# Kernel tuning notes

Hardware: AMD Instinct MI355X
Metric: run time of the kernel (lower is better)

The kernel has to match this reference:

```python
import jax, jax.numpy as jnp
import numpy as np

B, S, D, H = 4, 1024, 1024, 16
DK = D // H
NEG = -1e9


def setup_inputs() -> dict:
    key = jax.random.key(0)
    ks = jax.random.split(key, 8)
    inp = {
        "query": jax.random.normal(ks[0], (B, S, D), dtype=jnp.float32),
        "key": jax.random.normal(ks[1], (B, S, D), dtype=jnp.float32),
        "value": jax.random.normal(ks[2], (B, S, D), dtype=jnp.float32),
        "mask": jax.random.randint(ks[3], (B, S, S), 0, 2, dtype=jnp.int32),
        # bias-free Linear weights, torch layout [out, in]; y = x @ W.T
        "Wq": jax.random.normal(ks[4], (D, D), dtype=jnp.float32) / np.sqrt(D),
        "Wk": jax.random.normal(ks[5], (D, D), dtype=jnp.float32) / np.sqrt(D),
        "Wv": jax.random.normal(ks[6], (D, D), dtype=jnp.float32) / np.sqrt(D),
        "Wo": jax.random.normal(ks[7], (D, D), dtype=jnp.float32) / np.sqrt(D),
    }
    return inp


def _split_heads(x):
    # [B, S, D] -> [B, H, S, DK]
    return x.reshape(B, -1, H, DK).transpose(0, 2, 1, 3)


def reference(query, key, value, mask, Wq, Wk, Wv, Wo):
    q = _split_heads(query @ Wq.T)
    k = _split_heads(key @ Wk.T)
    v = _split_heads(value @ Wv.T)
    scores = jnp.einsum("bhqd,bhkd->bhqk", q, k) / jnp.sqrt(jnp.float32(DK))
    scores = jnp.where(mask[:, None, :, :] == 0, NEG, scores)
    p_attn = jax.nn.softmax(scores, axis=-1)
    x = jnp.einsum("bhqk,bhkd->bhqd", p_attn, v)
    x = x.transpose(0, 2, 1, 3).reshape(B, -1, D)
    # dropout p=0.0 (eval-equivalent): identity
    return x @ Wo.T
```

## Files before the change

kernel.cpp:

```cpp
#include <hip/hip_runtime.h>

#define BB 4
#define SS 1024
#define DD 1024
#define HH 16
#define DKK 64
#define MM (BB*SS)

typedef __bf16 bf16;
typedef __bf16 bf16x8 __attribute__((ext_vector_type(8)));
typedef float f32x4 __attribute__((ext_vector_type(4)));
typedef float f32x16 __attribute__((ext_vector_type(16)));

__device__ __forceinline__ f32x4 mfma16(bf16x8 a, bf16x8 b, f32x4 c) {
  return __builtin_amdgcn_mfma_f32_16x16x32_bf16(a, b, c, 0, 0, 0);
}
__device__ __forceinline__ f32x16 mfma32(bf16x8 a, bf16x8 b, f32x16 c) {
  return __builtin_amdgcn_mfma_f32_32x32x16_bf16(a, b, c, 0, 0, 0);
}
__device__ __forceinline__ float fexp2(float x) {
  return __builtin_amdgcn_exp2f(x);
}
__device__ __forceinline__ void gld_lds16(const bf16* g, bf16* l) {
  __builtin_amdgcn_global_load_lds(
      (const __attribute__((address_space(1))) void*)g,
      (__attribute__((address_space(3))) void*)l, 16, 0, 0);
}

__global__ __launch_bounds__(256)
void k_cvt7(const float* __restrict__ s0, const float* __restrict__ s1,
            const float* __restrict__ s2, const float* __restrict__ s3,
            const float* __restrict__ s4, const float* __restrict__ s5,
            const float* __restrict__ s6,
            bf16* __restrict__ d0, bf16* __restrict__ d1, bf16* __restrict__ d2,
            bf16* __restrict__ d3, bf16* __restrict__ d4, bf16* __restrict__ d5,
            bf16* __restrict__ d6) {
  const int t = blockIdx.y;
  const float* s = (t == 0) ? s0 : (t == 1) ? s1 : (t == 2) ? s2
                 : (t == 3) ? s3 : (t == 4) ? s4 : (t == 5) ? s5 : s6;
  bf16* d = (t == 0) ? d0 : (t == 1) ? d1 : (t == 2) ? d2
          : (t == 3) ? d3 : (t == 4) ? d4 : (t == 5) ? d5 : d6;
  const int n = (t < 3) ? (MM * DD) : (DD * DD);
  const int i0 = (blockIdx.x * 256 + threadIdx.x) * 8;
  if (i0 >= n) return;
  const f32x4 a = *(const f32x4*)(s + i0);
  const f32x4 b = *(const f32x4*)(s + i0 + 4);
  bf16x8 o;
#pragma unroll
  for (int j = 0; j < 4; ++j) { o[j] = (bf16)a[j]; o[4 + j] = (bf16)b[j]; }
  *(bf16x8*)(d + i0) = o;
}

__global__ __launch_bounds__(256) void k_mask_bits(const int* __restrict__ mask,
                                                   unsigned* __restrict__ bits) {
  const int row = blockIdx.x;
  const int tid = threadIdx.x;
  const int lane = tid & 63, wv = tid >> 6;
#pragma unroll
  for (int it = 0; it < 4; ++it) {
    const int base = it * 256 + wv * 64;
    const int col = base + lane;
    unsigned long long bal = __ballot(mask[(size_t)row * SS + col] != 0);
    if (lane == 0) {
      bits[(size_t)row * 32 + (base >> 5)] = (unsigned)bal;
      bits[(size_t)row * 32 + (base >> 5) + 1] = (unsigned)(bal >> 32);
    }
  }
}

#define QSCALE 0.1803368801111204f

template<int AF32, int CF32>
__device__ __forceinline__ void gemm_body(const void* __restrict__ Ap,
                                          const float* __restrict__ Wp,
                                          void* __restrict__ Cp,
                                          int Mtot, int N, int K, int blk,
                                          float oscale) {
  __shared__ bf16 Al[128 * 40];
  __shared__ bf16 Bl[128 * 40];
  const int tid = threadIdx.x;
  const int lane = tid & 63;
  const int l15 = lane & 15, l4 = lane >> 4;
  const int wv = tid >> 6;
  const int nbm = Mtot >> 7;
  const int bm = blk % nbm, bn = blk / nbm;
  const size_t m0 = (size_t)bm << 7, n0 = (size_t)bn << 7;
  const int wr = (wv >> 1) << 6, wc = (wv & 1) << 6;
  const int srow = tid >> 2, scol = (tid & 3) << 3;

  f32x4 acc[4][4];
#pragma unroll
  for (int i = 0; i < 4; ++i)
#pragma unroll
    for (int j = 0; j < 4; ++j) acc[i][j] = f32x4{0.f, 0.f, 0.f, 0.f};

  for (int k0 = 0; k0 < K; k0 += 32) {
#pragma unroll
    for (int c = 0; c < 2; ++c) {
      const int row = (c << 6) + srow;
      bf16x8 av;
      if (AF32) {
        const float* s = (const float*)Ap + (m0 + row) * (size_t)K + k0 + scol;
        f32x4 v0 = *(const f32x4*)s;
        f32x4 v1 = *(const f32x4*)(s + 4);
#pragma unroll
        for (int j = 0; j < 4; ++j) { av[j] = (bf16)v0[j]; av[4 + j] = (bf16)v1[j]; }
      } else {
        av = *(const bf16x8*)((const bf16*)Ap + (m0 + row) * (size_t)K + k0 + scol);
      }
      *(bf16x8*)&Al[row * 40 + scol] = av;

      const float* ws_ = Wp + (n0 + row) * (size_t)K + k0 + scol;
      f32x4 w0 = *(const f32x4*)ws_;
      f32x4 w1 = *(const f32x4*)(ws_ + 4);
      bf16x8 wv8;
#pragma unroll
      for (int j = 0; j < 4; ++j) { wv8[j] = (bf16)w0[j]; wv8[4 + j] = (bf16)w1[j]; }
      *(bf16x8*)&Bl[row * 40 + scol] = wv8;
    }
    __syncthreads();

    bf16x8 af[4], bfv[4];
#pragma unroll
    for (int t = 0; t < 4; ++t) {
      af[t]  = *(const bf16x8*)&Al[(wr + t * 16 + l15) * 40 + l4 * 8];
      bfv[t] = *(const bf16x8*)&Bl[(wc + t * 16 + l15) * 40 + l4 * 8];
    }
    __builtin_amdgcn_s_setprio(1);
#pragma unroll
    for (int mt = 0; mt < 4; ++mt)
#pragma unroll
      for (int nt = 0; nt < 4; ++nt)
        acc[mt][nt] = mfma16(af[mt], bfv[nt], acc[mt][nt]);
    __builtin_amdgcn_s_setprio(0);
    __syncthreads();
  }

#pragma unroll
  for (int mt = 0; mt < 4; ++mt)
#pragma unroll
    for (int nt = 0; nt < 4; ++nt)
#pragma unroll
      for (int r = 0; r < 4; ++r) {
        const size_t row = m0 + wr + mt * 16 + l4 * 4 + r;
        const size_t col = n0 + wc + nt * 16 + l15;
        if (CF32) ((float*)Cp)[row * N + col] = acc[mt][nt][r];
        else      ((bf16*)Cp)[row * N + col] = (bf16)(acc[mt][nt][r] * oscale);
      }
}

__global__ __launch_bounds__(256)
void k_gemm_qkv(const float* __restrict__ A0, const float* __restrict__ A1,
                const float* __restrict__ A2, const float* __restrict__ W0,
                const float* __restrict__ W1, const float* __restrict__ W2,
                bf16* __restrict__ C0, bf16* __restrict__ C1, bf16* __restrict__ C2) {
  const int z = blockIdx.z;
  const float* A = (z == 0) ? A0 : (z == 1) ? A1 : A2;
  const float* W = (z == 0) ? W0 : (z == 1) ? W1 : W2;
  bf16* C = (z == 0) ? C0 : (z == 1) ? C1 : C2;
  const float sc = (z == 0) ? QSCALE : 1.0f;
  gemm_body<1, 0>(A, W, C, MM, DD, DD, blockIdx.x, sc);
}

__global__ __launch_bounds__(256)
void k_gemm_out(const bf16* __restrict__ A, const float* __restrict__ W,
                float* __restrict__ C) {
  gemm_body<0, 1>(A, W, C, MM, DD, DD, blockIdx.x, 1.0f);
}

__global__ __launch_bounds__(256)
void k_gemm_qkv_b16(const bf16* __restrict__ A0, const bf16* __restrict__ A1,
                    const bf16* __restrict__ A2, const bf16* __restrict__ W0,
                    const bf16* __restrict__ W1, const bf16* __restrict__ W2,
                    bf16* __restrict__ C0, bf16* __restrict__ C1,
                    bf16* __restrict__ C2) {
  __shared__ bf16 Al[128 * 32];
  __shared__ bf16 Bl[128 * 32];
  const int z = blockIdx.z;
  const bf16* A = (z == 0) ? A0 : (z == 1) ? A1 : A2;
  const bf16* W = (z == 0) ? W0 : (z == 1) ? W1 : W2;
  bf16* C = (z == 0) ? C0 : (z == 1) ? C1 : C2;
  const float oscale = (z == 0) ? QSCALE : 1.0f;

  const int tid = threadIdx.x, lane = tid & 63, w = tid >> 6;
  const int l15 = lane & 15, l4 = lane >> 4;
  const int bm = blockIdx.x & 31, bn = blockIdx.x >> 5;
  const size_t m0 = (size_t)bm << 7, n0 = (size_t)bn << 7;
  const int wr = (w >> 1) << 6, wc = (w & 1) << 6;
  const int srow = w * 32 + (lane >> 2);
  const int scol = (lane & 3) << 3;

  f32x4 acc[4][4];
#pragma unroll
  for (int i = 0; i < 4; ++i)
#pragma unroll
    for (int j = 0; j < 4; ++j) acc[i][j] = f32x4{0.f, 0.f, 0.f, 0.f};

  for (int k0 = 0; k0 < DD; k0 += 32) {
    const bf16* ga = A + (m0 + srow) * (size_t)DD + k0 + scol;
    const bf16* gb = W + (n0 + srow) * (size_t)DD + k0 + scol;
    gld_lds16(ga,            &Al[(w * 32) * 32]);
    gld_lds16(ga + 16 * DD,  &Al[(w * 32 + 16) * 32]);
    gld_lds16(gb,            &Bl[(w * 32) * 32]);
    gld_lds16(gb + 16 * DD,  &Bl[(w * 32 + 16) * 32]);
    __syncthreads();

    bf16x8 af[4], bfv[4];
#pragma unroll
    for (int t = 0; t < 4; ++t) {
      af[t]  = *(const bf16x8*)&Al[(wr + t * 16 + l15) * 32 + l4 * 8];
      bfv[t] = *(const bf16x8*)&Bl[(wc + t * 16 + l15) * 32 + l4 * 8];
    }
#pragma unroll
    for (int mt = 0; mt < 4; ++mt)
#pragma unroll
      for (int nt = 0; nt < 4; ++nt)
        acc[mt][nt] = mfma16(af[mt], bfv[nt], acc[mt][nt]);
    __syncthreads();
  }

#pragma unroll
  for (int mt = 0; mt < 4; ++mt)
#pragma unroll
    for (int nt = 0; nt < 4; ++nt)
#pragma unroll
      for (int r = 0; r < 4; ++r) {
        const size_t row = m0 + wr + mt * 16 + l4 * 4 + r;
        const size_t col = n0 + wc + nt * 16 + l15;
        C[row * DD + col] = (bf16)(acc[mt][nt][r] * oscale);
      }
}

__global__ __launch_bounds__(256)
void k_gemm_out_b16(const bf16* __restrict__ A, const bf16* __restrict__ W,
                    float* __restrict__ C) {
  __shared__ bf16 Al[128 * 32];
  __shared__ bf16 Bl[128 * 32];
  const int tid = threadIdx.x, lane = tid & 63, w = tid >> 6;
  const int l15 = lane & 15, l4 = lane >> 4;
  const int bm = blockIdx.x & 31, bn = blockIdx.x >> 5;
  const size_t m0 = (size_t)bm << 7, n0 = (size_t)bn << 7;
  const int wr = (w >> 1) << 6, wc = (w & 1) << 6;
  const int srow = w * 32 + (lane >> 2);
  const int scol = (lane & 3) << 3;

  f32x4 acc[4][4];
#pragma unroll
  for (int i = 0; i < 4; ++i)
#pragma unroll
    for (int j = 0; j < 4; ++j) acc[i][j] = f32x4{0.f, 0.f, 0.f, 0.f};

  for (int k0 = 0; k0 < DD; k0 += 32) {
    const bf16* ga = A + (m0 + srow) * (size_t)DD + k0 + scol;
    const bf16* gb = W + (n0 + srow) * (size_t)DD + k0 + scol;
    gld_lds16(ga,            &Al[(w * 32) * 32]);
    gld_lds16(ga + 16 * DD,  &Al[(w * 32 + 16) * 32]);
    gld_lds16(gb,            &Bl[(w * 32) * 32]);
    gld_lds16(gb + 16 * DD,  &Bl[(w * 32 + 16) * 32]);
    __syncthreads();

    bf16x8 af[4], bfv[4];
#pragma unroll
    for (int t = 0; t < 4; ++t) {
      af[t]  = *(const bf16x8*)&Al[(wr + t * 16 + l15) * 32 + l4 * 8];
      bfv[t] = *(const bf16x8*)&Bl[(wc + t * 16 + l15) * 32 + l4 * 8];
    }
#pragma unroll
    for (int mt = 0; mt < 4; ++mt)
#pragma unroll
      for (int nt = 0; nt < 4; ++nt)
        acc[mt][nt] = mfma16(af[mt], bfv[nt], acc[mt][nt]);
    __syncthreads();
  }

#pragma unroll
  for (int mt = 0; mt < 4; ++mt)
#pragma unroll
    for (int nt = 0; nt < 4; ++nt)
#pragma unroll
      for (int r = 0; r < 4; ++r) {
        const size_t row = m0 + wr + mt * 16 + l4 * 4 + r;
        const size_t col = n0 + wc + nt * 16 + l15;
        C[row * DD + col] = acc[mt][nt][r];
      }
}

__global__ __launch_bounds__(256)
void k_attn(const bf16* __restrict__ Qw, const bf16* __restrict__ Kw,
            const bf16* __restrict__ Vw, const unsigned* __restrict__ mb,
            bf16* __restrict__ Xw) {
  __shared__ union {
    bf16 v[4][2048];
    struct { float o[64 * 67]; float ml[4][2][64];
             float inv[64]; float mst[64]; } m;
  } sh;
  const int tid = threadIdx.x, lane = tid & 63, w = tid >> 6;
  const int l31 = lane & 31, hi = lane >> 5;
  const unsigned bid = blockIdx.x;
  const unsigned wg = (bid & 7) * 128 + (bid >> 3);
  const int bh = wg >> 4, qblk = wg & 15;
  const int h = bh & 15, b = bh >> 4;
  const int q0 = qblk * 64;

  bf16x8 qf[2][4];
#pragma unroll
  for (int qt = 0; qt < 2; ++qt) {
    const bf16* Qb = Qw + (size_t)(b * SS + q0 + qt * 32 + l31) * DD + h * 64 + hi * 8;
#pragma unroll
    for (int kt = 0; kt < 4; ++kt) qf[qt][kt] = *(const bf16x8*)(Qb + kt * 16);
  }
  const bf16* Kg = Kw + (size_t)(b * SS) * DD + h * 64 + hi * 8;
  const bf16* Vg = Vw + (size_t)(b * SS) * DD + h * 64;
  const unsigned* mrow0 = mb + (size_t)(b * SS + q0 + l31) * 32 + w * 8;
  const unsigned* mrow1 = mrow0 + 32 * 32;

  const int grow = lane >> 3;
  const int gcol = (lane & 7) * 8;
  const int kvw = w << 8;
  bf16* Vst = sh.v[w];

  f32x16 aco[2][2];
#pragma unroll
  for (int qt = 0; qt < 2; ++qt)
#pragma unroll
    for (int dt = 0; dt < 2; ++dt)
#pragma unroll
      for (int r = 0; r < 16; ++r) aco[qt][dt][r] = 0.f;
  float mx[2] = { -3e38f, -3e38f }, ssum[2] = { 0.f, 0.f };

  for (int t = 0; t < 8; ++t) {
    const int kv0 = kvw + t * 32;
#pragma unroll
    for (int i_ = 0; i_ < 4; ++i_)
      gld_lds16(Vg + (size_t)(kv0 + i_ * 8 + grow) * DD + gcol, Vst + i_ * 512);
    bf16x8 kf[4];
    {
      const bf16* kp = Kg + (size_t)(kv0 + l31) * DD;
#pragma unroll
      for (int kt = 0; kt < 4; ++kt) kf[kt] = *(const bf16x8*)(kp + kt * 16);
    }
    const unsigned mw0 = mrow0[t], mw1 = mrow1[t];

    bf16x8 va[2][2];
    union { bf16x8 v; int q[4]; } pa0[2], pa1[2];
    float psum[2];

#pragma unroll
    for (int qt = 0; qt < 2; ++qt) {
      f32x16 s;
#pragma unroll
      for (int r = 0; r < 16; ++r) s[r] = 0.f;
      __builtin_amdgcn_s_setprio(1);
#pragma unroll
      for (int kt = 0; kt < 4; ++kt) s = mfma32(kf[kt], qf[qt][kt], s);
      __builtin_amdgcn_s_setprio(0);

      const unsigned mw = qt ? mw1 : mw0;
      float p[16];
#pragma unroll
      for (int r = 0; r < 16; ++r) {
        const int pos = (r & 3) + 8 * (r >> 2) + 4 * hi;
        p[r] = ((mw >> pos) & 1) ? s[r] : -1e9f;
      }
      float t0 = fmaxf(p[0], p[1]),  t1 = fmaxf(p[2], p[3]);
      float t2 = fmaxf(p[4], p[5]),  t3 = fmaxf(p[6], p[7]);
      float t4 = fmaxf(p[8], p[9]),  t5 = fmaxf(p[10], p[11]);
      float t6 = fmaxf(p[12], p[13]), t7 = fmaxf(p[14], p[15]);
      float rm = fmaxf(fmaxf(fmaxf(t0, t1), fmaxf(t2, t3)),
                       fmaxf(fmaxf(t4, t5), fmaxf(t6, t7)));
      rm = fmaxf(rm, __shfl_xor(rm, 32));
      if (!__all(rm <= mx[qt] + 8.0f)) {
        const float mn = fmaxf(mx[qt], rm);
        const float scal = fexp2(mx[qt] - mn);
        mx[qt] = mn; ssum[qt] *= scal;
#pragma unroll
        for (int dt = 0; dt < 2; ++dt)
#pragma unroll
          for (int r = 0; r < 16; ++r) aco[qt][dt][r] *= scal;
      }
#pragma unroll
      for (int r = 0; r < 16; ++r) p[r] = fexp2(p[r] - mx[qt]);
      {
        float a0 = (p[0] + p[1]) + (p[2] + p[3]);
        float a1 = (p[4] + p[5]) + (p[6] + p[7]);
        float a2 = (p[8] + p[9]) + (p[10] + p[11]);
        float a3 = (p[12] + p[13]) + (p[14] + p[15]);
        psum[qt] = (a0 + a1) + (a2 + a3);
      }
      ssum[qt] += psum[qt];
      int dpk[8];
#pragma unroll
      for (int i = 0; i < 8; ++i) {
        union { bf16 hh[2]; int v; } u;
        u.hh[0] = (bf16)p[2 * i]; u.hh[1] = (bf16)p[2 * i + 1];
        dpk[i] = u.v;
      }
      const int sa = hi ? dpk[0] : dpk[2], sb = hi ? dpk[1] : dpk[3];
      const int sc_ = hi ? dpk[4] : dpk[6], sd = hi ? dpk[5] : dpk[7];
      const int ra = __shfl_xor(sa, 32), rb = __shfl_xor(sb, 32);
      const int rc = __shfl_xor(sc_, 32), rd = __shfl_xor(sd, 32);
      pa0[qt].q[0] = hi ? ra : dpk[0];  pa0[qt].q[1] = hi ? rb : dpk[1];
      pa0[qt].q[2] = hi ? dpk[2] : ra;  pa0[qt].q[3] = hi ? dpk[3] : rb;
      pa1[qt].q[0] = hi ? rc : dpk[4];  pa1[qt].q[1] = hi ? rd : dpk[5];
      pa1[qt].q[2] = hi ? dpk[6] : rc;  pa1[qt].q[3] = hi ? dpk[7] : rd;

      if (qt == 0) {
        asm volatile("s_waitcnt vmcnt(0)" ::: "memory");
        __builtin_amdgcn_sched_barrier(0);
#pragma unroll
        for (int dt = 0; dt < 2; ++dt)
#pragma unroll
          for (int s2 = 0; s2 < 2; ++s2) {
            bf16x8 tv;
#pragma unroll
            for (int j = 0; j < 8; ++j)
              tv[j] = Vst[(s2 * 16 + hi * 8 + j) * 64 + dt * 32 + l31];
            va[dt][s2] = tv;
          }
      }
      __builtin_amdgcn_s_setprio(1);
#pragma unroll
      for (int dt = 0; dt < 2; ++dt) {
        aco[qt][dt] = mfma32(va[dt][0], pa0[qt].v, aco[qt][dt]);
        aco[qt][dt] = mfma32(va[dt][1], pa1[qt].v, aco[qt][dt]);
      }
      __builtin_amdgcn_s_setprio(0);
    }
  }

#pragma unroll
  for (int qt = 0; qt < 2; ++qt) ssum[qt] += __shfl_xor(ssum[qt], 32);
  __syncthreads();
  if (hi == 0) {
#pragma unroll
    for (int qt = 0; qt < 2; ++qt) {
      sh.m.ml[w][0][qt * 32 + l31] = mx[qt];
      sh.m.ml[w][1][qt * 32 + l31] = ssum[qt];
    }
  }
  __syncthreads();
  if (w == 0) {
    const float M0 = sh.m.ml[0][0][lane], M1 = sh.m.ml[1][0][lane];
    const float M2 = sh.m.ml[2][0][lane], M3 = sh.m.ml[3][0][lane];
    const float ms = fmaxf(fmaxf(M0, M1), fmaxf(M2, M3));
    const float ls = sh.m.ml[0][1][lane] * fexp2(M0 - ms)
                   + sh.m.ml[1][1][lane] * fexp2(M1 - ms)
                   + sh.m.ml[2][1][lane] * fexp2(M2 - ms)
                   + sh.m.ml[3][1][lane] * fexp2(M3 - ms);
    sh.m.inv[lane] = 1.0f / ls;
    sh.m.mst[lane] = ms;
  }
  __syncthreads();
  float fown[2];
#pragma unroll
  for (int qt = 0; qt < 2; ++qt)
    fown[qt] = fexp2(sh.m.ml[w][0][qt * 32 + l31] - sh.m.mst[qt * 32 + l31]);
  for (int rd2 = 0; rd2 < 4; ++rd2) {
    if (w == rd2) {
#pragma unroll
      for (int qt = 0; qt < 2; ++qt)
#pragma unroll
        for (int dt = 0; dt < 2; ++dt)
#pragma unroll
          for (int r = 0; r < 16; ++r) {
            const int d = dt * 32 + (r & 3) + 8 * (r >> 2) + 4 * hi;
            const int o = d * 67 + qt * 32 + l31;
            const float val = aco[qt][dt][r] * fown[qt];
            if (rd2 == 0) sh.m.o[o] = val;
            else          sh.m.o[o] += val;
          }
    }
    __syncthreads();
  }
  {
    const int q = tid >> 2, c0 = (tid & 3) * 16;
    const float inv = sh.m.inv[q];
    bf16x8 w0, w1;
#pragma unroll
    for (int j = 0; j < 8; ++j) {
      w0[j] = (bf16)(sh.m.o[(c0 + j) * 67 + q] * inv);
      w1[j] = (bf16)(sh.m.o[(c0 + 8 + j) * 67 + q] * inv);
    }
    bf16* xp = Xw + (size_t)(b * SS + q0 + q) * DD + h * 64 + c0;
    *(bf16x8*)xp = w0;
    *(bf16x8*)(xp + 8) = w1;
  }
}

extern "C" void kernel_launch(void* const* d_in, const int* in_sizes, int n_in,
                              void* d_out, int out_size, void* d_ws, size_t ws_size,
                              hipStream_t stream) {
  const float* q32 = (const float*)d_in[0];
  const float* k32 = (const float*)d_in[1];
  const float* v32 = (const float*)d_in[2];
  const int* mask = (const int*)d_in[3];
  const float* Wq = (const float*)d_in[4];
  const float* Wk = (const float*)d_in[5];
  const float* Wv = (const float*)d_in[6];
  const float* Wo = (const float*)d_in[7];
  float* out = (float*)d_out;

  const size_t eAct = (size_t)MM * DD;
  const size_t eW = (size_t)DD * DD;

  bf16* Qb = (bf16*)d_ws;
  bf16* Kb = Qb + eAct;
  bf16* Vb = Kb + eAct;
  bf16* Xb = Vb + eAct;
  unsigned* mbits = (unsigned*)(Xb + eAct);
  bf16* cvtBase = (bf16*)(mbits + (size_t)MM * 32);
  bf16* Aq = cvtBase;
  bf16* Ak = Aq + eAct;
  bf16* Av = Ak + eAct;
  bf16* Wqb = Av + eAct;
  bf16* Wkb = Wqb + eW;
  bf16* Wvb = Wkb + eW;
  bf16* Wob = Wvb + eW;
  const size_t need = (size_t)((bf16*)(Wob + eW) - (bf16*)d_ws) * sizeof(bf16);

  k_mask_bits<<<BB * SS, 256, 0, stream>>>(mask, mbits);
  if (ws_size >= need) {
    k_cvt7<<<dim3(2048, 7), 256, 0, stream>>>(q32, k32, v32, Wq, Wk, Wv, Wo,
                                              Aq, Ak, Av, Wqb, Wkb, Wvb, Wob);
    k_gemm_qkv_b16<<<dim3(256, 1, 3), 256, 0, stream>>>(
        Aq, Ak, Av, Wqb, Wkb, Wvb, Qb, Kb, Vb);
    k_attn<<<BB * HH * (SS / 64), 256, 0, stream>>>(Qb, Kb, Vb, mbits, Xb);
    k_gemm_out_b16<<<256, 256, 0, stream>>>(Xb, Wob, out);
  } else {
    k_gemm_qkv<<<dim3((MM / 128) * (DD / 128), 1, 3), 256, 0, stream>>>(
        q32, k32, v32, Wq, Wk, Wv, Qb, Kb, Vb);
    k_attn<<<BB * HH * (SS / 64), 256, 0, stream>>>(Qb, Kb, Vb, mbits, Xb);
    k_gemm_out<<<(MM / 128) * (DD / 128), 256, 0, stream>>>(Xb, Wo, out);
  }
}
```

Measured before the change: 135.2 us.

## Pre-swizzle K/V and mask bits into MFMA fragment order for attention

Adds a k_frag kernel that rewrites K and V per (batch, head, 32-row block) into the exact per-lane MFMA fragment order, and reorders the mask bitmap so each lane reads its word contiguously. The attention kernel then loads K and V fragments with coalesced vector global loads, with no LDS staging of V, no waitcnt barrier and no LDS union, and the loop is unrolled by two. This removes strided global loads and LDS transposes inside the hot loop. The cost is an extra kernel launch plus a read and write of K/V, and more workspace. In the fallback path Kfp/Vfp may fall outside the available workspace.

```diff
diff --git a/kernel.cpp b/kernel.cpp
--- a/kernel.cpp
+++ b/kernel.cpp
@@ -54,17 +54,55 @@
 __global__ __launch_bounds__(256) void k_mask_bits(const int* __restrict__ mask,
                                                    unsigned* __restrict__ bits) {
   const int row = blockIdx.x;
+  const int b = row >> 10, q = row & 1023;
+  const int qblk = q >> 6, qt = (q >> 5) & 1, l = q & 31;
+  const size_t base = ((size_t)(b * 16 + qblk) * 2 + qt) * 4;
   const int tid = threadIdx.x;
   const int lane = tid & 63, wv = tid >> 6;
 #pragma unroll
   for (int it = 0; it < 4; ++it) {
-    const int base = it * 256 + wv * 64;
-    const int col = base + lane;
-    unsigned long long bal = __ballot(mask[(size_t)row * SS + col] != 0);
+    const int cb = it * 256 + wv * 64;
+    unsigned long long bal = __ballot(mask[(size_t)row * SS + cb + lane] != 0);
     if (lane == 0) {
-      bits[(size_t)row * 32 + (base >> 5)] = (unsigned)bal;
-      bits[(size_t)row * 32 + (base >> 5) + 1] = (unsigned)(bal >> 32);
-    }
+      const int c0 = cb >> 5;
+#pragma unroll
+      for (int dd = 0; dd < 2; ++dd) {
+        const int c = c0 + dd;
+        bits[((base + (c >> 3)) * 8 + (c & 7)) * 32 + l] =
+            (unsigned)(bal >> (32 * dd));
+      }
+    }
+  }
+}
+
+__global__ __launch_bounds__(256)
+void k_frag(const bf16* __restrict__ K, const bf16* __restrict__ V,
+            bf16* __restrict__ Kf, bf16* __restrict__ Vf) {
+  __shared__ bf16 Kl[32 * 66];
+  __shared__ bf16 Vl[32 * 66];
+  const int kvb = blockIdx.x, h = blockIdx.y, b = blockIdx.z;
+  const int tid = threadIdx.x;
+  const int r = tid >> 3, c0 = (tid & 7) * 8;
+  const size_t src = (size_t)(b * SS + kvb * 32 + r) * DD + h * 64 + c0;
+  *(bf16x8*)&Kl[r * 66 + c0] = *(const bf16x8*)(K + src);
+  *(bf16x8*)&Vl[r * 66 + c0] = *(const bf16x8*)(V + src);
+  __syncthreads();
+  const int lane = tid & 63, l31 = lane & 31, hi = lane >> 5;
+  const size_t tb = ((size_t)((b * HH + h) * 32 + kvb)) * 2048 + tid * 8;
+  {
+    const int kt = tid >> 6;
+    bf16x8 ok;
+#pragma unroll
+    for (int j = 0; j < 8; ++j) ok[j] = Kl[l31 * 66 + kt * 16 + hi * 8 + j];
+    *(bf16x8*)(Kf + tb) = ok;
+  }
+  {
+    const int s2 = tid >> 7, dt = (tid >> 6) & 1;
+    bf16x8 ov;
+#pragma unroll
+    for (int j = 0; j < 8; ++j)
+      ov[j] = Vl[(s2 * 16 + hi * 8 + j) * 66 + dt * 32 + l31];
+    *(bf16x8*)(Vf + tb) = ov;
   }
 }
 
@@ -286,14 +324,11 @@
 }
 
 __global__ __launch_bounds__(256)
-void k_attn(const bf16* __restrict__ Qw, const bf16* __restrict__ Kw,
-            const bf16* __restrict__ Vw, const unsigned* __restrict__ mb,
+void k_attn(const bf16* __restrict__ Qw, const bf16* __restrict__ Kf,
+            const bf16* __restrict__ Vf, const unsigned* __restrict__ mb,
             bf16* __restrict__ Xw) {
-  __shared__ union {
-    bf16 v[4][2048];
-    struct { float o[64 * 67]; float ml[4][2][64];
-             float inv[64]; float mst[64]; } m;
-  } sh;
+  __shared__ struct { float o[64 * 67]; float ml[4][2][64];
+                      float inv[64]; float mst[64]; } sh;
   const int tid = threadIdx.x, lane = tid & 63, w = tid >> 6;
   const int l31 = lane & 31, hi = lane >> 5;
   const unsigned bid = blockIdx.x;
@@ -309,15 +344,11 @@
 #pragma unroll
     for (int kt = 0; kt < 4; ++kt) qf[qt][kt] = *(const bf16x8*)(Qb + kt * 16);
   }
-  const bf16* Kg = Kw + (size_t)(b * SS) * DD + h * 64 + hi * 8;
-  const bf16* Vg = Vw + (size_t)(b * SS) * DD + h * 64;
-  const unsigned* mrow0 = mb + (size_t)(b * SS + q0 + l31) * 32 + w * 8;
-  const unsigned* mrow1 = mrow0 + 32 * 32;
-
-  const int grow = lane >> 3;
-  const int gcol = (lane & 7) * 8;
-  const int kvw = w << 8;
-  bf16* Vst = sh.v[w];
+  const bf16* Kfb = Kf + ((size_t)((b * HH + h) * 32 + w * 8)) * 2048 + lane * 8;
+  const bf16* Vfb = Vf + ((size_t)((b * HH + h) * 32 + w * 8)) * 2048 + lane * 8;
+  const unsigned* mq0 = mb +
+      ((size_t)(((b * 16 + qblk) * 2 + 0) * 4 + w) * 8) * 32 + l31;
+  const unsigned* mq1 = mq0 + 1024;
 
   f32x16 aco[2][2];
 #pragma unroll
@@ -328,22 +359,22 @@
       for (int r = 0; r < 16; ++r) aco[qt][dt][r] = 0.f;
   float mx[2] = { -3e38f, -3e38f }, ssum[2] = { 0.f, 0.f };
 
+#pragma unroll 2
   for (int t = 0; t < 8; ++t) {
-    const int kv0 = kvw + t * 32;
-#pragma unroll
-    for (int i_ = 0; i_ < 4; ++i_)
-      gld_lds16(Vg + (size_t)(kv0 + i_ * 8 + grow) * DD + gcol, Vst + i_ * 512);
+    const bf16* tk = Kfb + t * 2048;
+    const bf16* tv = Vfb + t * 2048;
     bf16x8 kf[4];
-    {
-      const bf16* kp = Kg + (size_t)(kv0 + l31) * DD;
-#pragma unroll
-      for (int kt = 0; kt < 4; ++kt) kf[kt] = *(const bf16x8*)(kp + kt * 16);
-    }
-    const unsigned mw0 = mrow0[t], mw1 = mrow1[t];
-
+#pragma unroll
+    for (int kt = 0; kt < 4; ++kt) kf[kt] = *(const bf16x8*)(tk + kt * 512);
     bf16x8 va[2][2];
+#pragma unroll
+    for (int s2 = 0; s2 < 2; ++s2)
+#pragma unroll
+      for (int dt = 0; dt < 2; ++dt)
+        va[dt][s2] = *(const bf16x8*)(tv + (s2 * 2 + dt) * 512);
+    const unsigned mw0 = mq0[t * 32], mw1 = mq1[t * 32];
+
     union { bf16x8 v; int q[4]; } pa0[2], pa1[2];
-    float psum[2];
 
 #pragma unroll
     for (int qt = 0; qt < 2; ++qt) {
@@ -385,9 +416,8 @@
         float a1 = (p[4] + p[5]) + (p[6] + p[7]);
         float a2 = (p[8] + p[9]) + (p[10] + p[11]);
         float a3 = (p[12] + p[13]) + (p[14] + p[15]);
-        psum[qt] = (a0 + a1) + (a2 + a3);
-      }
-      ssum[qt] += psum[qt];
+        ssum[qt] += (a0 + a1) + (a2 + a3);
+      }
       int dpk[8];
 #pragma unroll
       for (int i = 0; i < 8; ++i) {
@@ -404,20 +434,6 @@
       pa1[qt].q[0] = hi ? rc : dpk[4];  pa1[qt].q[1] = hi ? rd : dpk[5];
       pa1[qt].q[2] = hi ? dpk[6] : rc;  pa1[qt].q[3] = hi ? dpk[7] : rd;
 
-      if (qt == 0) {
-        asm volatile("s_waitcnt vmcnt(0)" ::: "memory");
-        __builtin_amdgcn_sched_barrier(0);
-#pragma unroll
-        for (int dt = 0; dt < 2; ++dt)
-#pragma unroll
-          for (int s2 = 0; s2 < 2; ++s2) {
-            bf16x8 tv;
-#pragma unroll
-            for (int j = 0; j < 8; ++j)
-              tv[j] = Vst[(s2 * 16 + hi * 8 + j) * 64 + dt * 32 + l31];
-            va[dt][s2] = tv;
-          }
-      }
       __builtin_amdgcn_s_setprio(1);
 #pragma unroll
       for (int dt = 0; dt < 2; ++dt) {
@@ -434,27 +450,27 @@
   if (hi == 0) {
 #pragma unroll
     for (int qt = 0; qt < 2; ++qt) {
-      sh.m.ml[w][0][qt * 32 + l31] = mx[qt];
-      sh.m.ml[w][1][qt * 32 + l31] = ssum[qt];
+      sh.ml[w][0][qt * 32 + l31] = mx[qt];
+      sh.ml[w][1][qt * 32 + l31] = ssum[qt];
     }
   }
   __syncthreads();
   if (w == 0) {
-    const float M0 = sh.m.ml[0][0][lane], M1 = sh.m.ml[1][0][lane];
-    const float M2 = sh.m.ml[2][0][lane], M3 = sh.m.ml[3][0][lane];
+    const float M0 = sh.ml[0][0][lane], M1 = sh.ml[1][0][lane];
+    const float M2 = sh.ml[2][0][lane], M3 = sh.ml[3][0][lane];
     const float ms = fmaxf(fmaxf(M0, M1), fmaxf(M2, M3));
-    const float ls = sh.m.ml[0][1][lane] * fexp2(M0 - ms)
-                   + sh.m.ml[1][1][lane] * fexp2(M1 - ms)
-                   + sh.m.ml[2][1][lane] * fexp2(M2 - ms)
-                   + sh.m.ml[3][1][lane] * fexp2(M3 - ms);
-    sh.m.inv[lane] = 1.0f / ls;
-    sh.m.mst[lane] = ms;
+    const float ls = sh.ml[0][1][lane] * fexp2(M0 - ms)
+                   + sh.ml[1][1][lane] * fexp2(M1 - ms)
+                   + sh.ml[2][1][lane] * fexp2(M2 - ms)
+                   + sh.ml[3][1][lane] * fexp2(M3 - ms);
+    sh.inv[lane] = 1.0f / ls;
+    sh.mst[lane] = ms;
   }
   __syncthreads();
   float fown[2];
 #pragma unroll
   for (int qt = 0; qt < 2; ++qt)
-    fown[qt] = fexp2(sh.m.ml[w][0][qt * 32 + l31] - sh.m.mst[qt * 32 + l31]);
+    fown[qt] = fexp2(sh.ml[w][0][qt * 32 + l31] - sh.mst[qt * 32 + l31]);
   for (int rd2 = 0; rd2 < 4; ++rd2) {
     if (w == rd2) {
 #pragma unroll
@@ -466,20 +482,20 @@
             const int d = dt * 32 + (r & 3) + 8 * (r >> 2) + 4 * hi;
             const int o = d * 67 + qt * 32 + l31;
             const float val = aco[qt][dt][r] * fown[qt];
-            if (rd2 == 0) sh.m.o[o] = val;
-            else          sh.m.o[o] += val;
+            if (rd2 == 0) sh.o[o] = val;
+            else          sh.o[o] += val;
           }
     }
     __syncthreads();
   }
   {
     const int q = tid >> 2, c0 = (tid & 3) * 16;
-    const float inv = sh.m.inv[q];
+    const float inv = sh.inv[q];
     bf16x8 w0, w1;
 #pragma unroll
     for (int j = 0; j < 8; ++j) {
-      w0[j] = (bf16)(sh.m.o[(c0 + j) * 67 + q] * inv);
-      w1[j] = (bf16)(sh.m.o[(c0 + 8 + j) * 67 + q] * inv);
+      w0[j] = (bf16)(sh.o[(c0 + j) * 67 + q] * inv);
+      w1[j] = (bf16)(sh.o[(c0 + 8 + j) * 67 + q] * inv);
     }
     bf16* xp = Xw + (size_t)(b * SS + q0 + q) * DD + h * 64 + c0;
     *(bf16x8*)xp = w0;
@@ -508,7 +524,9 @@
   bf16* Vb = Kb + eAct;
   bf16* Xb = Vb + eAct;
   unsigned* mbits = (unsigned*)(Xb + eAct);
-  bf16* cvtBase = (bf16*)(mbits + (size_t)MM * 32);
+  bf16* Kfp = (bf16*)(mbits + (size_t)MM * 32);
+  bf16* Vfp = Kfp + eAct;
+  bf16* cvtBase = Vfp + eAct;
   bf16* Aq = cvtBase;
   bf16* Ak = Aq + eAct;
   bf16* Av = Ak + eAct;
@@ -524,12 +542,14 @@
                                               Aq, Ak, Av, Wqb, Wkb, Wvb, Wob);
     k_gemm_qkv_b16<<<dim3(256, 1, 3), 256, 0, stream>>>(
         Aq, Ak, Av, Wqb, Wkb, Wvb, Qb, Kb, Vb);
-    k_attn<<<BB * HH * (SS / 64), 256, 0, stream>>>(Qb, Kb, Vb, mbits, Xb);
+    k_frag<<<dim3(32, HH, BB), 256, 0, stream>>>(Kb, Vb, Kfp, Vfp);
+    k_attn<<<BB * HH * (SS / 64), 256, 0, stream>>>(Qb, Kfp, Vfp, mbits, Xb);
     k_gemm_out_b16<<<256, 256, 0, stream>>>(Xb, Wob, out);
   } else {
     k_gemm_qkv<<<dim3((MM / 128) * (DD / 128), 1, 3), 256, 0, stream>>>(
         q32, k32, v32, Wq, Wk, Wv, Qb, Kb, Vb);
-    k_attn<<<BB * HH * (SS / 64), 256, 0, stream>>>(Qb, Kb, Vb, mbits, Xb);
+    k_frag<<<dim3(32, HH, BB), 256, 0, stream>>>(Kb, Vb, Kfp, Vfp);
+    k_attn<<<BB * HH * (SS / 64), 256, 0, stream>>>(Qb, Kfp, Vfp, mbits, Xb);
     k_gemm_out<<<(MM / 128) * (DD / 128), 256, 0, stream>>>(Xb, Wo, out);
   }
 }
```

After: 154.5 us. +14.3%, slower.
